# Performance work log

Measured on AMD Instinct MI355X. Metric: run time of the kernel, lower is better.

The kernel has to match this reference:

```python
import jax, jax.numpy as jnp
import numpy as np

B, S, D, H, O = 128, 1024, 64, 512, 1


def setup_inputs() -> dict:
    key = jax.random.key(0)
    ks = jax.random.split(key, 16)
    sc = 1.0 / np.sqrt(H)
    u = lambda k, shape: jax.random.uniform(k, shape, jnp.float32, -sc, sc)
    return {
        "x": jax.random.normal(ks[0], (B, S, D), jnp.float32),
        "W_ih0": u(ks[1], (4 * H, D)), "W_hh0": u(ks[2], (4 * H, H)),
        "b_ih0": u(ks[3], (4 * H,)), "b_hh0": u(ks[4], (4 * H,)),
        "W_ih1": u(ks[5], (4 * H, H)), "W_hh1": u(ks[6], (4 * H, H)),
        "b_ih1": u(ks[7], (4 * H,)), "b_hh1": u(ks[8], (4 * H,)),
        "W_a": u(ks[9], (H, H)), "b_a": u(ks[10], (H,)),
        "v_a": u(ks[11], (1, H)), "b_v": u(ks[12], (1,)),
        "fc_W": u(ks[13], (O, H)), "fc_b": u(ks[14], (O,)),
    }


def lstm_layer(x_sbd, W_ih, W_hh, b_ih, b_hh):
    # x_sbd: [S, B, Din] -> outputs [S, B, H]; PyTorch gate order i,f,g,o
    h0 = jnp.zeros((x_sbd.shape[1], W_hh.shape[1]), x_sbd.dtype)

    def step(carry, x_t):
        h, c = carry
        g = x_t @ W_ih.T + b_ih + h @ W_hh.T + b_hh
        i, f, gg, o = jnp.split(g, 4, axis=-1)
        c = jax.nn.sigmoid(f) * c + jax.nn.sigmoid(i) * jnp.tanh(gg)
        h = jax.nn.sigmoid(o) * jnp.tanh(c)
        return (h, c), h

    _, hs = jax.lax.scan(step, (h0, h0), x_sbd)
    return hs


def entmax15(x):
    # x: [B, S], normalization over axis 1 (faithful to the source's variant)
    n = x.shape[1]
    x = x - jnp.max(x, axis=1, keepdims=True)
    xs = jnp.flip(jnp.sort(x, axis=1), axis=1)  # descending
    csm = jnp.cumsum(xs, axis=1)
    rhos = jnp.arange(1, n + 1, dtype=x.dtype)
    support = rhos * xs - csm + 0.5
    support_thresh = support / rhos
    ssize = jnp.clip(jnp.sum(support > 0, axis=1, keepdims=True), 1, n - 1)
    tau = jnp.take_along_axis(support_thresh, ssize, axis=1)
    d = x - tau
    pos = d > 0
    y = jnp.where(pos, jnp.sqrt(jnp.where(pos, d, 1.0)), 0.0)
    return y / jnp.sum(y, axis=1, keepdims=True)


def reference(x, W_ih0, W_hh0, b_ih0, b_hh0, W_ih1, W_hh1, b_ih1, b_hh1,
              W_a, b_a, v_a, b_v, fc_W, fc_b):
    x_sbd = jnp.transpose(x, (1, 0, 2))  # [S, B, D]
    h1 = lstm_layer(x_sbd, W_ih0, W_hh0, b_ih0, b_hh0)
    h2 = lstm_layer(h1, W_ih1, W_hh1, b_ih1, b_hh1)
    lstm_out = jnp.transpose(h2, (1, 0, 2))  # [B, S, H]
    # additive attention energies: v_a(tanh(W_a(h)))
    e = jnp.einsum('bsh,oh->bso', jnp.tanh(jnp.einsum('bsh,gh->bsg', lstm_out, W_a) + b_a), v_a) + b_v
    att_weights = entmax15(e[..., 0])  # [B, S]
    context = jnp.einsum('bs,bsh->bh', att_weights, lstm_out)
    # dropout is identity in eval mode
    output = context @ fc_W.T + fc_b  # [B, O]
    return output, att_weights
```

## Files before the change

### kernel.cpp

```cpp
#include <hip/hip_runtime.h>

typedef __attribute__((ext_vector_type(8))) _Float16 half8;
typedef __attribute__((ext_vector_type(4))) float f32x4;
typedef __attribute__((ext_vector_type(4))) int   i32x4;

#define DEV static __device__ __forceinline__

DEV i32x4 mfma8i(i32x4 a, i32x4 b, i32x4 c){
  return __builtin_amdgcn_mfma_i32_16x16x64_i8(a, b, c, 0, 0, 0);
}
DEV void ld4(i32x4& d, const char* p){
  asm volatile("global_load_dwordx4 %0, %1, off sc0 sc1" : "=v"(d) : "v"(p));
}
DEV void st1(char* p, int v){
  asm volatile("global_store_byte %0, %1, off sc0 sc1" :: "v"(p), "v"(v) : "memory");
}
DEV void st_flag(unsigned int* p, unsigned int v){
  asm volatile("s_waitcnt vmcnt(0)" ::: "memory");
  asm volatile("global_store_dword %0, %1, off sc0 sc1" :: "v"(p), "v"(v) : "memory");
}
DEV void drain_vm(){ asm volatile("s_waitcnt vmcnt(0)" ::: "memory"); }
DEV void poll_ge(unsigned int* fp, unsigned int tgt){
  for (;;){
    unsigned int v = __hip_atomic_load(fp, __ATOMIC_RELAXED, __HIP_MEMORY_SCOPE_AGENT);
    if (__all(v >= tgt)) break;
    __builtin_amdgcn_s_sleep(1);
  }
}

DEV void str_h(const i32x4* W, const i32x4* B, i32x4* G){
  G[0]=mfma8i(W[0],B[0],G[0]);
  G[1]=mfma8i(W[0],B[1],G[1]); G[1]=mfma8i(W[1],B[0],G[1]);
  G[2]=mfma8i(W[0],B[2],G[2]); G[2]=mfma8i(W[1],B[1],G[2]); G[2]=mfma8i(W[2],B[0],G[2]);
  G[3]=mfma8i(W[0],B[3],G[3]); G[3]=mfma8i(W[1],B[2],G[3]); G[3]=mfma8i(W[2],B[1],G[3]); G[3]=mfma8i(W[3],B[0],G[3]);
  G[4]=mfma8i(W[0],B[4],G[4]); G[4]=mfma8i(W[1],B[3],G[4]); G[4]=mfma8i(W[2],B[2],G[4]); G[4]=mfma8i(W[3],B[1],G[4]); G[4]=mfma8i(W[4],B[0],G[4]);
  G[5]=mfma8i(W[1],B[4],G[5]); G[5]=mfma8i(W[2],B[3],G[5]); G[5]=mfma8i(W[3],B[2],G[5]); G[5]=mfma8i(W[4],B[1],G[5]);
}
DEV void str_x(const i32x4* W, const i32x4* X, i32x4* G){
  G[0]=mfma8i(W[0],X[0],G[0]);
  G[1]=mfma8i(W[0],X[1],G[1]); G[1]=mfma8i(W[1],X[0],G[1]);
  G[2]=mfma8i(W[0],X[2],G[2]); G[2]=mfma8i(W[1],X[1],G[2]); G[2]=mfma8i(W[2],X[0],G[2]);
  G[3]=mfma8i(W[0],X[3],G[3]); G[3]=mfma8i(W[1],X[2],G[3]); G[3]=mfma8i(W[2],X[1],G[3]); G[3]=mfma8i(W[3],X[0],G[3]);
  G[4]=mfma8i(W[0],X[4],G[4]); G[4]=mfma8i(W[1],X[3],G[4]); G[4]=mfma8i(W[2],X[2],G[4]); G[4]=mfma8i(W[3],X[1],G[4]); G[4]=mfma8i(W[4],X[0],G[4]);
  G[5]=mfma8i(W[0],X[5],G[5]); G[5]=mfma8i(W[1],X[4],G[5]); G[5]=mfma8i(W[2],X[3],G[5]); G[5]=mfma8i(W[3],X[2],G[5]); G[5]=mfma8i(W[4],X[1],G[5]);
}

#define SEG_STRIDE 4352
#define NSEG 20
#define LDS_BYTES  (NSEG * SEG_STRIDE)

DEV void stage_issue(char* const* hp, size_t tbase, i32x4* v, int tid){
  const int row = tid >> 4;
  const int off = (tid & 15) * 16;
  #pragma unroll
  for (int u = 0; u < NSEG; ++u){
    int plane = u >> 2, tile = (u >> 1) & 1, half = u & 1;
    ld4(v[u], hp[plane] + tbase + (size_t)(tile * 16 + row) * 512 + (size_t)half * 256 + off);
  }
}
DEV void stage_write(const i32x4* v, char* lds, int tid){
  const int row = tid >> 4;
  const int off = (tid & 15) * 16;
  #pragma unroll
  for (int u = 0; u < NSEG; ++u)
    *(i32x4*)(lds + u * SEG_STRIDE + row * 272 + off) = v[u];
}

DEV void compute_full(const char* const* wp, size_t rowb, int wofs,
                      const char* lds, int l15, int l4, i32x4* Ga, i32x4* Gb){
  #pragma unroll
  for (int c = 0; c < 8; ++c){
    const int half = c >> 2, cc = c & 3;
    i32x4 Wc[5], Ba[5], Bb[5];
    #pragma unroll
    for (int p = 0; p < 5; ++p)
      Wc[p] = *(const i32x4*)(wp[p] + rowb + (size_t)(wofs + c) * 64 + l4 * 16);
    #pragma unroll
    for (int p = 0; p < 5; ++p){
      Ba[p] = *(const i32x4*)(lds + (p * 4 + 0 + half) * SEG_STRIDE + l15 * 272 + cc * 64 + l4 * 16);
      Bb[p] = *(const i32x4*)(lds + (p * 4 + 2 + half) * SEG_STRIDE + l15 * 272 + cc * 64 + l4 * 16);
    }
    str_h(Wc, Ba, Ga);
    str_h(Wc, Bb, Gb);
  }
}

__global__ void k_prep_zero(unsigned int* cnt){
  cnt[threadIdx.x] = 0u;
}

DEV void wsplit5(float v, char* o1, char* o2, char* o3, char* o4, char* o5){
  float q1 = rintf(v * 0x1p11f);
  float r1 = fmaf(q1, -0x1p-11f, v);
  float q2 = rintf(r1 * 0x1p18f);
  float r2 = fmaf(q2, -0x1p-18f, r1);
  float q3 = rintf(r2 * 0x1p25f);
  float r3 = fmaf(q3, -0x1p-25f, r2);
  float q4 = rintf(r3 * 0x1p32f);
  float r4 = fmaf(q4, -0x1p-32f, r3);
  float q5 = rintf(r4 * 0x1p39f);
  *o1=(char)(int)q1; *o2=(char)(int)q2; *o3=(char)(int)q3;
  *o4=(char)(int)q4; *o5=(char)(int)q5;
}

__global__ void k_prep_w0(const float* __restrict__ Wih0, const float* __restrict__ Whh0,
                          char* __restrict__ p1, char* __restrict__ p2, char* __restrict__ p3,
                          char* __restrict__ p4, char* __restrict__ p5){
  int idx = blockIdx.x * 256 + threadIdx.x;
  int k = idx % 576;
  int r = (idx / 576) & 63;
  int j = idx / 36864;
  int R = (r & 3) * 512 + j * 16 + (r >> 2);
  float v = (k < 512) ? Whh0[(size_t)R * 512 + k] : Wih0[(size_t)R * 64 + (k - 512)];
  wsplit5(v, p1 + idx, p2 + idx, p3 + idx, p4 + idx, p5 + idx);
}

__global__ void k_prep_w1(const float* __restrict__ Wih1, const float* __restrict__ Whh1,
                          char* __restrict__ p1, char* __restrict__ p2, char* __restrict__ p3,
                          char* __restrict__ p4, char* __restrict__ p5){
  int idx = blockIdx.x * 256 + threadIdx.x;
  int k = idx & 1023;
  int r = (idx >> 10) & 63;
  int j = idx >> 16;
  int R = (r & 3) * 512 + j * 16 + (r >> 2);
  float v = (k < 512) ? Wih1[(size_t)R * 512 + k] : Whh1[(size_t)R * 512 + (k - 512)];
  wsplit5(v, p1 + idx, p2 + idx, p3 + idx, p4 + idx, p5 + idx);
}

__global__ void k_prep_b(const float* __restrict__ bih0, const float* __restrict__ bhh0,
                         const float* __restrict__ bih1, const float* __restrict__ bhh1,
                         double* __restrict__ bias0, double* __restrict__ bias1){
  int idx = blockIdx.x * 256 + threadIdx.x;
  int i2 = idx & 2047;
  int j = i2 >> 6, r = i2 & 63;
  int R = (r & 3) * 512 + j * 16 + (r >> 2);
  if (idx < 2048) bias0[i2] = (double)bih0[R] + (double)bhh0[R];
  else            bias1[i2] = (double)bih1[R] + (double)bhh1[R];
}

__global__ void k_prep_wa(const float* __restrict__ Wa,
                          char* __restrict__ p1, char* __restrict__ p2,
                          char* __restrict__ p3, char* __restrict__ p4){
  int idx = blockIdx.x * 256 + threadIdx.x;
  float v = Wa[idx];
  float q1 = rintf(v * 0x1p11f);
  float r1 = fmaf(q1, -0x1p-11f, v);
  float q2 = rintf(r1 * 0x1p18f);
  float r2 = fmaf(q2, -0x1p-18f, r1);
  float q3 = rintf(r2 * 0x1p25f);
  float r3 = fmaf(q3, -0x1p-25f, r2);
  float q4 = rintf(r3 * 0x1p32f);
  p1[idx]=(char)(int)q1; p2[idx]=(char)(int)q2;
  p3[idx]=(char)(int)q3; p4[idx]=(char)(int)q4;
}

DEV void hsplit5(double hd, char* o1, char* o2, char* o3, char* o4, char* o5){
  double q1 = rint(hd * 64.0);
  double r1 = hd - q1 * 0x1p-6;
  double q2 = rint(r1 * 0x1p13);
  double r2 = r1 - q2 * 0x1p-13;
  double q3 = rint(r2 * 0x1p20);
  double r3 = r2 - q3 * 0x1p-20;
  double q4 = rint(r3 * 0x1p27);
  double r4 = r3 - q4 * 0x1p-27;
  double q5 = rint(r4 * 0x1p34);
  *o1=(char)(int)q1; *o2=(char)(int)q2; *o3=(char)(int)q3;
  *o4=(char)(int)q4; *o5=(char)(int)q5;
}

DEV double sigd(double xv){ return 1.0 / (1.0 + exp(-xv)); }

__constant__ double SH_[6] = {0x1p-17, 0x1p-24, 0x1p-31, 0x1p-38, 0x1p-45, 0x1p-52};
__constant__ double SX_[6] = {0x1p-13, 0x1p-20, 0x1p-27, 0x1p-34, 0x1p-41, 0x1p-48};

__global__ __launch_bounds__(256, 1) void k_lstm_fused(
    const float* __restrict__ x,
    const char* w0p1, const char* w0p2, const char* w0p3, const char* w0p4, const char* w0p5,
    const double* __restrict__ bias0,
    const char* w1p1, const char* w1p2, const char* w1p3, const char* w1p4, const char* w1p5,
    const double* __restrict__ bias1,
    char* h1a, char* h1b, char* h1c, char* h1d, char* h1e,
    char* h2a, char* h2b, char* h2c, char* h2d, char* h2e,
    _Float16* __restrict__ h2h, char* __restrict__ h2l8,
    unsigned int* __restrict__ cnt)
{
  __shared__ char sbuf[LDS_BYTES];
  const int wg   = blockIdx.x;
  const int tid  = threadIdx.x;
  const int w    = tid >> 6;
  const int lane = tid & 63;
  const int l15  = lane & 15;
  const int l4   = lane >> 4;
  unsigned int* pflagL0 = cnt;
  unsigned int* pflagH2 = cnt + 128;

  const int isL1 = wg >= 128;
  const int wgl  = isL1 ? wg - 128 : wg;
  const int gi   = wgl >> 5;
  const int j    = wgl & 31;
  const int r0   = w * 16 + l15;
  const int b0   = gi * 32 + l15;
  const int b1   = b0 + 16;
  const int hid  = j * 16 + w * 4 + l4;
  const size_t ringmt0 = (size_t)b0 * 512;
  const size_t ringmt1 = (size_t)b1 * 512;
  const size_t gbase   = (size_t)(gi * 32) * 512;

  char* h1p[5] = {h1a, h1b, h1c, h1d, h1e};
  char* h2p[5] = {h2a, h2b, h2c, h2d, h2e};
  const i32x4 z = {0,0,0,0};

  if (!isL1){
    const char* wp[5] = {w0p1, w0p2, w0p3, w0p4, w0p5};
    const size_t rowb = ((size_t)j * 64 + r0) * 576;
    i32x4 WX[5];
    #pragma unroll
    for (int p = 0; p < 5; ++p)
      WX[p] = *(const i32x4*)(wp[p] + rowb + 8 * 64 + l4 * 16);
    double bsd[4];
    #pragma unroll
    for (int q = 0; q < 4; ++q) bsd[q] = bias0[j * 64 + w * 16 + l4 * 4 + q];
    double c0 = 0.0, c1 = 0.0;

    for (int t = 0; t < 1024; ++t){
      i32x4 XA[6], XB[6];
      {
        #pragma unroll
        for (int mt = 0; mt < 2; ++mt){
          const float* xr = x + ((size_t)(mt ? b1 : b0) * 1024 + t) * 64 + l4 * 16;
          unsigned int a[6][4] = {{0,0,0,0},{0,0,0,0},{0,0,0,0},{0,0,0,0},{0,0,0,0},{0,0,0,0}};
          #pragma unroll
          for (int i = 0; i < 16; ++i){
            float v = xr[i];
            float q1 = rintf(v * 4.0f);
            float r1 = fmaf(q1, -0.25f, v);
            float q2 = rintf(r1 * 0x1p9f);
            float r2 = fmaf(q2, -0x1p-9f, r1);
            float q3 = rintf(r2 * 0x1p16f);
            float r3 = fmaf(q3, -0x1p-16f, r2);
            float q4 = rintf(r3 * 0x1p23f);
            float r4 = fmaf(q4, -0x1p-23f, r3);
            float q5 = rintf(r4 * 0x1p30f);
            float r5 = fmaf(q5, -0x1p-30f, r4);
            float q6 = rintf(r5 * 0x1p37f);
            int wi = i >> 2, sh = (i & 3) * 8;
            a[0][wi] |= ((unsigned)(unsigned char)(char)(int)q1) << sh;
            a[1][wi] |= ((unsigned)(unsigned char)(char)(int)q2) << sh;
            a[2][wi] |= ((unsigned)(unsigned char)(char)(int)q3) << sh;
            a[3][wi] |= ((unsigned)(unsigned char)(char)(int)q4) << sh;
            a[4][wi] |= ((unsigned)(unsigned char)(char)(int)q5) << sh;
            a[5][wi] |= ((unsigned)(unsigned char)(char)(int)q6) << sh;
          }
          i32x4* X = mt ? XB : XA;
          #pragma unroll
          for (int p = 0; p < 6; ++p)
            X[p] = i32x4{(int)a[p][0], (int)a[p][1], (int)a[p][2], (int)a[p][3]};
        }
      }
      i32x4 Gha[6], Ghb[6], Gxa[6], Gxb[6];
      #pragma unroll
      for (int k = 0; k < 6; ++k){ Gha[k]=z; Ghb[k]=z; Gxa[k]=z; Gxb[k]=z; }
      str_x(WX, XA, Gxa);
      str_x(WX, XB, Gxb);

      if (w == 0){
        unsigned int* fp = (lane < 32) ? (pflagL0 + gi * 32 + lane)
                                       : (pflagH2 + gi * 32 + (lane - 32));
        unsigned int tgt = (lane < 32) ? (unsigned)t
                          : ((t >= 8) ? (unsigned)(t - 7) : 0u);
        poll_ge(fp, tgt);
      }
      __syncthreads();

      if (t > 0){
        i32x4 A[NSEG];
        const size_t sb = ((size_t)((t - 1) & 7) << 16) + gbase;
        stage_issue(h1p, sb, A, tid);
        drain_vm();
        __builtin_amdgcn_sched_barrier(0);
        stage_write(A, sbuf, tid);
        __syncthreads();
        compute_full(wp, rowb, 0, sbuf, l15, l4, Gha, Ghb);
      }

      const size_t rb = (size_t)(t & 7) << 16;
      #pragma unroll
      for (int mt = 0; mt < 2; ++mt){
        i32x4* Gh = mt ? Ghb : Gha;
        i32x4* Gx = mt ? Gxb : Gxa;
        double g[4];
        #pragma unroll
        for (int q = 0; q < 4; ++q){
          double s = bsd[q];
          #pragma unroll
          for (int k = 0; k < 6; ++k)
            s += (double)Gh[k][q] * SH_[k] + (double)Gx[k][q] * SX_[k];
          g[q] = s;
        }
        double& cs = mt ? c1 : c0;
        cs = sigd(g[1]) * cs + sigd(g[0]) * tanh(g[2]);
        double hv = sigd(g[3]) * tanh(cs);
        size_t o = rb + (mt ? ringmt1 : ringmt0) + hid;
        char v1c, v2c, v3c, v4c, v5c;
        hsplit5(hv, &v1c, &v2c, &v3c, &v4c, &v5c);
        st1(h1p[0] + o, v1c); st1(h1p[1] + o, v2c); st1(h1p[2] + o, v3c);
        st1(h1p[3] + o, v4c); st1(h1p[4] + o, v5c);
      }

      drain_vm();
      __syncthreads();
      if (tid == 0) st_flag(pflagL0 + wgl, (unsigned)(t + 1));
    }
  } else {
    const char* wp[5] = {w1p1, w1p2, w1p3, w1p4, w1p5};
    const size_t rowb = ((size_t)j * 64 + r0) * 1024;
    double bsd[4];
    #pragma unroll
    for (int q = 0; q < 4; ++q) bsd[q] = bias1[j * 64 + w * 16 + l4 * 4 + q];
    double c0 = 0.0, c1 = 0.0;

    for (int t = 0; t < 1024; ++t){
      if (w == 0){
        unsigned int* fp = (lane < 32) ? (pflagL0 + gi * 32 + lane)
                                       : (pflagH2 + gi * 32 + (lane - 32));
        unsigned int tgt = (lane < 32) ? (unsigned)(t + 1)
                          : ((t > 0) ? (unsigned)t : 0u);
        poll_ge(fp, tgt);
      }
      __syncthreads();

      i32x4 Gha[6], Ghb[6];
      #pragma unroll
      for (int k = 0; k < 6; ++k){ Gha[k]=z; Ghb[k]=z; }

      i32x4 A[NSEG], Bv[NSEG];
      const size_t sbA = ((size_t)(t & 7) << 16) + gbase;
      stage_issue(h1p, sbA, A, tid);
      if (t > 0){
        const size_t sbB = ((size_t)((t - 1) & 3) << 16) + gbase;
        stage_issue(h2p, sbB, Bv, tid);
        asm volatile("s_waitcnt vmcnt(20)" ::: "memory");
      } else {
        drain_vm();
      }
      __builtin_amdgcn_sched_barrier(0);
      stage_write(A, sbuf, tid);
      __syncthreads();
      compute_full(wp, rowb, 0, sbuf, l15, l4, Gha, Ghb);
      __syncthreads();

      if (t > 0){
        drain_vm();
        __builtin_amdgcn_sched_barrier(0);
        stage_write(Bv, sbuf, tid);
        __syncthreads();
        compute_full(wp, rowb, 8, sbuf, l15, l4, Gha, Ghb);
      }

      const size_t rb = (size_t)(t & 3) << 16;
      #pragma unroll
      for (int mt = 0; mt < 2; ++mt){
        i32x4* Gh = mt ? Ghb : Gha;
        double g[4];
        #pragma unroll
        for (int q = 0; q < 4; ++q){
          double s = bsd[q];
          #pragma unroll
          for (int k = 0; k < 6; ++k) s += (double)Gh[k][q] * SH_[k];
          g[q] = s;
        }
        double& cs = mt ? c1 : c0;
        cs = sigd(g[1]) * cs + sigd(g[0]) * tanh(g[2]);
        double hv = sigd(g[3]) * tanh(cs);
        size_t o = rb + (mt ? ringmt1 : ringmt0) + hid;
        char v1c, v2c, v3c, v4c, v5c;
        hsplit5(hv, &v1c, &v2c, &v3c, &v4c, &v5c);
        st1(h2p[0] + o, v1c); st1(h2p[1] + o, v2c); st1(h2p[2] + o, v3c);
        st1(h2p[3] + o, v4c); st1(h2p[4] + o, v5c);
        float hf = (float)hv;
        _Float16 hh = (_Float16)hf;
        float rs = hf - (float)hh;
        union { _Float16 h; unsigned short u; } cb; cb.h = hh;
        int E = (cb.u >> 10) & 31; if (E < 1) E = 1;
        int qr = (int)rintf(ldexpf(rs, 33 - E));
        qr = qr < -127 ? -127 : (qr > 127 ? 127 : qr);
        size_t pb = ((size_t)(mt ? b1 : b0) * 1024 + t) * 512 + hid;
        h2h[pb] = hh;
        h2l8[pb] = (char)qr;
      }

      drain_vm();
      __syncthreads();
      if (tid == 0) st_flag(pflagH2 + wgl, (unsigned)(t + 1));
    }
  }
}

__global__ __launch_bounds__(256) void k_att_e(
    const _Float16* __restrict__ h2, const char* __restrict__ h2l8,
    const char* __restrict__ wa1, const char* __restrict__ wa2,
    const char* __restrict__ wa3, const char* __restrict__ wa4,
    const float* __restrict__ b_a, const float* __restrict__ v_a,
    const float* __restrict__ b_v, double* __restrict__ e)
{
  __shared__ char Ap[4][32][528];
  __shared__ char Wp[2][4][16][528];
  __shared__ double partial[2][32];
  const int tid  = threadIdx.x;
  const int w    = tid >> 6;
  const int mt   = w & 1;
  const int nh   = w >> 1;
  const int lane = tid & 63;
  const int l15  = lane & 15;
  const int l4   = lane >> 4;
  const size_t rid0 = (size_t)blockIdx.x * 32;

  for (int i = tid; i < 2048; i += 256){
    int row = i >> 6, c8 = (i & 63) << 3;
    const _Float16* hp = h2 + (rid0 + row) * 512 + c8;
    const char*     rp = h2l8 + (rid0 + row) * 512 + c8;
    unsigned long long o1 = 0, o2 = 0, o3 = 0, o4 = 0;
    #pragma unroll
    for (int q = 0; q < 8; ++q){
      union { _Float16 h; unsigned short u; } cb; cb.h = hp[q];
      int E = (cb.u >> 10) & 31; if (E < 1) E = 1;
      float h = (float)cb.h + ldexpf((float)rp[q], E - 33);
      float q1 = rintf(h * 64.f);     float r1 = fmaf(q1, -0x1p-6f, h);
      float q2 = rintf(r1 * 0x1p13f); float r2 = fmaf(q2, -0x1p-13f, r1);
      float q3 = rintf(r2 * 0x1p20f); float r3 = fmaf(q3, -0x1p-20f, r2);
      float q4 = rintf(r3 * 0x1p27f);
      o1 |= ((unsigned long long)(unsigned char)(char)(int)q1) << (8 * q);
      o2 |= ((unsigned long long)(unsigned char)(char)(int)q2) << (8 * q);
      o3 |= ((unsigned long long)(unsigned char)(char)(int)q3) << (8 * q);
      o4 |= ((unsigned long long)(unsigned char)(char)(int)q4) << (8 * q);
    }
    *(unsigned long long*)&Ap[0][row][c8] = o1;
    *(unsigned long long*)&Ap[1][row][c8] = o2;
    *(unsigned long long*)&Ap[2][row][c8] = o3;
    *(unsigned long long*)&Ap[3][row][c8] = o4;
  }
  __syncthreads();

  const int sh = tid >> 7;
  const int st = tid & 127;
  double ep0 = 0.0, ep1 = 0.0, ep2 = 0.0, ep3 = 0.0;
  for (int it = 0; it < 16; ++it){
    if (it) __syncthreads();
    {
      int nt = sh * 16 + it;
      for (int i = st; i < 512; i += 128){
        int row = (i >> 5) & 15, c16 = (i & 31) << 4;
        size_t go = (size_t)(nt * 16 + row) * 512 + c16;
        *(i32x4*)&Wp[sh][0][row][c16] = *(const i32x4*)(wa1 + go);
        *(i32x4*)&Wp[sh][1][row][c16] = *(const i32x4*)(wa2 + go);
        *(i32x4*)&Wp[sh][2][row][c16] = *(const i32x4*)(wa3 + go);
        *(i32x4*)&Wp[sh][3][row][c16] = *(const i32x4*)(wa4 + go);
      }
    }
    __syncthreads();
    i32x4 G0={0,0,0,0},G1={0,0,0,0},G2={0,0,0,0},G3={0,0,0,0},G4={0,0,0,0},G5={0,0,0,0};
    #pragma unroll
    for (int c = 0; c < 8; ++c){
      int ko = c * 64 + l4 * 16;
      i32x4 A1 = *(const i32x4*)&Ap[0][mt * 16 + l15][ko];
      i32x4 A2 = *(const i32x4*)&Ap[1][mt * 16 + l15][ko];
      i32x4 A3 = *(const i32x4*)&Ap[2][mt * 16 + l15][ko];
      i32x4 A4 = *(const i32x4*)&Ap[3][mt * 16 + l15][ko];
      i32x4 B1 = *(const i32x4*)&Wp[nh][0][l15][ko];
      i32x4 B2 = *(const i32x4*)&Wp[nh][1][l15][ko];
      i32x4 B3 = *(const i32x4*)&Wp[nh][2][l15][ko];
      i32x4 B4 = *(const i32x4*)&Wp[nh][3][l15][ko];
      G0 = mfma8i(A1, B1, G0);
      G1 = mfma8i(A1, B2, G1); G1 = mfma8i(A2, B1, G1);
      G2 = mfma8i(A1, B3, G2); G2 = mfma8i(A2, B2, G2); G2 = mfma8i(A3, B1, G2);
      G3 = mfma8i(A1, B4, G3); G3 = mfma8i(A2, B3, G3); G3 = mfma8i(A3, B2, G3); G3 = mfma8i(A4, B1, G3);
      G4 = mfma8i(A2, B4, G4); G4 = mfma8i(A3, B3, G4); G4 = mfma8i(A4, B2, G4);
      G5 = mfma8i(A3, B4, G5); G5 = mfma8i(A4, B3, G5);
    }
    int n = (nh * 16 + it) * 16 + l15;
    double ban = (double)b_a[n], van = (double)v_a[n];
    #pragma unroll
    for (int q = 0; q < 4; ++q){
      double val = (double)G0[q]*SH_[0] + (double)G1[q]*SH_[1] + (double)G2[q]*SH_[2]
                 + (double)G3[q]*SH_[3] + (double)G4[q]*SH_[4] + (double)G5[q]*SH_[5] + ban;
      double tv = tanh(val) * van;
      if (q == 0) ep0 += tv; else if (q == 1) ep1 += tv;
      else if (q == 2) ep2 += tv; else ep3 += tv;
    }
  }
  #pragma unroll
  for (int m = 1; m < 16; m <<= 1){
    ep0 += __shfl_xor(ep0, m); ep1 += __shfl_xor(ep1, m);
    ep2 += __shfl_xor(ep2, m); ep3 += __shfl_xor(ep3, m);
  }
  if (l15 == 0){
    int rbase = mt * 16 + l4 * 4;
    partial[nh][rbase + 0] = ep0;
    partial[nh][rbase + 1] = ep1;
    partial[nh][rbase + 2] = ep2;
    partial[nh][rbase + 3] = ep3;
  }
  __syncthreads();
  if (tid < 32)
    e[rid0 + tid] = partial[0][tid] + partial[1][tid] + (double)b_v[0];
}

__global__ __launch_bounds__(256) void k_entmax(
    const double* __restrict__ e, const _Float16* __restrict__ h2,
    const float* __restrict__ fcW, const float* __restrict__ fcb,
    float* __restrict__ out)
{
  __shared__ double xu[1024], sbd[1024], t0d[1024], t1d[1024];
  __shared__ float sbf[1024];
  __shared__ float red4[4];
  __shared__ double redd[4];
  __shared__ double scald;
  const int tid  = threadIdx.x;
  const int b    = blockIdx.x;
  const int wv   = tid >> 6;
  const int lane = tid & 63;

  double lm = -1e300;
  for (int i = tid; i < 1024; i += 256){
    double v = e[b * 1024 + i];
    xu[i] = v;
    lm = fmax(lm, v);
  }
  for (int m = 32; m >= 1; m >>= 1) lm = fmax(lm, __shfl_xor(lm, m));
  if (lane == 0) redd[wv] = lm;
  __syncthreads();
  double rowmax = fmax(fmax(redd[0], redd[1]), fmax(redd[2], redd[3]));
  __syncthreads();
  for (int i = tid; i < 1024; i += 256){
    double v = xu[i] - rowmax;
    xu[i] = v; sbd[i] = v;
  }
  __syncthreads();

  for (int ksz = 2; ksz <= 1024; ksz <<= 1){
    for (int jj = ksz >> 1; jj > 0; jj >>= 1){
      for (int i = tid; i < 1024; i += 256){
        int ixj = i ^ jj;
        if (ixj > i){
          double a = sbd[i], c = sbd[ixj];
          if (((i & ksz) == 0) ? (a > c) : (a < c)){ sbd[i] = c; sbd[ixj] = a; }
        }
      }
      __syncthreads();
    }
  }

  for (int i = tid; i < 1024; i += 256) t0d[i] = sbd[1023 - i];
  __syncthreads();
  double* src = t0d; double* dst = t1d;
  for (int off = 1; off < 1024; off <<= 1){
    for (int i = tid; i < 1024; i += 256)
      dst[i] = src[i] + ((i >= off) ? src[i - off] : 0.0);
    __syncthreads();
    double* tmp = src; src = dst; dst = tmp;
  }

  float lc = 0.f;
  for (int i = tid; i < 1024; i += 256){
    double xs_i = sbd[1023 - i];
    double sup = (double)(i + 1) * xs_i - src[i] + 0.5;
    if (sup > 0.0) lc += 1.f;
  }
  for (int m = 32; m >= 1; m >>= 1) lc += __shfl_xor(lc, m);
  if (lane == 0) red4[wv] = lc;
  __syncthreads();
  if (tid == 0){
    int cntS = (int)(red4[0] + red4[1] + red4[2] + red4[3] + 0.5f);
    int ss = cntS < 1 ? 1 : (cntS > 1023 ? 1023 : cntS);
    double xss = sbd[1023 - ss];
    scald = ((double)(ss + 1) * xss - src[ss] + 0.5) / (double)(ss + 1);
  }
  __syncthreads();
  double tau = scald;

  double ls = 0.0;
  for (int i = tid; i < 1024; i += 256){
    double d = xu[i] - tau;
    double y = (d > 0.0) ? sqrt(d) : 0.0;
    dst[i] = y;
    ls += y;
  }
  for (int m = 32; m >= 1; m >>= 1) ls += __shfl_xor(ls, m);
  if (lane == 0) redd[wv] = ls;
  __syncthreads();
  double Z = redd[0] + redd[1] + redd[2] + redd[3];
  __syncthreads();
  for (int i = tid; i < 1024; i += 256){
    float a = (float)(dst[i] / Z);
    sbf[i] = a;
    out[128 + b * 1024 + i] = a;
  }
  __syncthreads();

  const int h0 = tid * 2;
  float cx0 = 0.f, cx1 = 0.f;
  for (int s = 0; s < 1024; ++s){
    float wt = sbf[s];
    if (wt > 0.f){
      unsigned int u = *(const unsigned int*)(h2 + ((size_t)b * 1024 + s) * 512 + h0);
      union { unsigned int u; _Float16 h[2]; } cv; cv.u = u;
      cx0 += wt * (float)cv.h[0];
      cx1 += wt * (float)cv.h[1];
    }
  }
  float p = fcW[h0] * cx0 + fcW[h0 + 1] * cx1;
  for (int m = 32; m >= 1; m >>= 1) p += __shfl_xor(p, m);
  if (lane == 0) red4[wv] = p;
  __syncthreads();
  if (tid == 0) out[b] = red4[0] + red4[1] + red4[2] + red4[3] + fcb[0];
}

extern "C" void kernel_launch(void* const* d_in, const int* in_sizes, int n_in,
                              void* d_out, int out_size, void* d_ws, size_t ws_size,
                              hipStream_t stream)
{
  (void)in_sizes; (void)n_in; (void)out_size;
  const float* x    = (const float*)d_in[0];
  const float* Wih0 = (const float*)d_in[1];
  const float* Whh0 = (const float*)d_in[2];
  const float* bih0 = (const float*)d_in[3];
  const float* bhh0 = (const float*)d_in[4];
  const float* Wih1 = (const float*)d_in[5];
  const float* Whh1 = (const float*)d_in[6];
  const float* bih1 = (const float*)d_in[7];
  const float* bhh1 = (const float*)d_in[8];
  const float* Wa   = (const float*)d_in[9];
  const float* ba   = (const float*)d_in[10];
  const float* va   = (const float*)d_in[11];
  const float* bv   = (const float*)d_in[12];
  const float* fcW  = (const float*)d_in[13];
  const float* fcb  = (const float*)d_in[14];

  const size_t NEED = 223773696ull;
  if (ws_size < NEED) return;

  char* ws = (char*)d_ws;
  unsigned int* cnt = (unsigned int*)(ws);
  char* w0p[5]; for (int p = 0; p < 5; ++p) w0p[p] = ws + 1024ull + (size_t)p * 1179648ull;
  double* bias0 = (double*)(ws + 5899264ull);
  char* w1p[5]; for (int p = 0; p < 5; ++p) w1p[p] = ws + 5915648ull + (size_t)p * 2097152ull;
  double* bias1 = (double*)(ws + 16401408ull);
  char* wa1 = ws + 16417792ull;
  char* wa2 = wa1 + 262144ull;
  char* wa3 = wa2 + 262144ull;
  char* wa4 = wa3 + 262144ull;
  char* h1p[5]; for (int p = 0; p < 5; ++p) h1p[p] = ws + 17466368ull + (size_t)p * 524288ull;
  char* h2p[5]; for (int p = 0; p < 5; ++p) h2p[p] = ws + 20087808ull + (size_t)p * 262144ull;
  double* ebuf = (double*)(ws + 21398528ull);
  _Float16* h2h = (_Float16*)(ws + 22447104ull);
  char* h2l8 = ws + 156664832ull;
  float* out = (float*)d_out;

  k_prep_zero<<<1, 256, 0, stream>>>(cnt);
  k_prep_w0<<<4608, 256, 0, stream>>>(Wih0, Whh0, w0p[0], w0p[1], w0p[2], w0p[3], w0p[4]);
  k_prep_w1<<<8192, 256, 0, stream>>>(Wih1, Whh1, w1p[0], w1p[1], w1p[2], w1p[3], w1p[4]);
  k_prep_b<<<16, 256, 0, stream>>>(bih0, bhh0, bih1, bhh1, bias0, bias1);
  k_prep_wa<<<1024, 256, 0, stream>>>(Wa, wa1, wa2, wa3, wa4);
  k_lstm_fused<<<256, 256, 0, stream>>>(x,
      w0p[0], w0p[1], w0p[2], w0p[3], w0p[4], bias0,
      w1p[0], w1p[1], w1p[2], w1p[3], w1p[4], bias1,
      h1p[0], h1p[1], h1p[2], h1p[3], h1p[4],
      h2p[0], h2p[1], h2p[2], h2p[3], h2p[4],
      h2h, h2l8, cnt);
  k_att_e<<<4096, 256, 0, stream>>>(h2h, h2l8, wa1, wa2, wa3, wa4, ba, va, bv, ebuf);
  k_entmax<<<128, 256, 0, stream>>>(ebuf, h2h, fcW, fcb, out);
}
```

Before: 19.41 ms.

## Repartition LSTM work: 16-batch groups, two gate tiles per wave sharing B-operand

Reassigns the persistent LSTM workgroups so each covers 16 batch rows (8 batch groups) and two 16-row weight tiles per wave, instead of 32 batch rows with one weight tile. Each LDS B fragment is now reused across two weight tiles, and the per-step staging of the hidden state halves (NSEG 20→10). Layer 0 now polls its dependency flags before doing the x-projection. The intent is to shrink per-step staging and LDS traffic and reduce the number of flags polled on the serial recurrence critical path. In exchange each wave loads twice as many weight fragments, and the layer-0 x-projection no longer overlaps the flag wait.

```diff
diff --git a/kernel.cpp b/kernel.cpp
--- a/kernel.cpp
+++ b/kernel.cpp
@@ -46,7 +46,7 @@
 }
 
 #define SEG_STRIDE 4352
-#define NSEG 20
+#define NSEG 10
 #define LDS_BYTES  (NSEG * SEG_STRIDE)
 
 DEV void stage_issue(char* const* hp, size_t tbase, i32x4* v, int tid){
@@ -54,8 +54,8 @@
   const int off = (tid & 15) * 16;
   #pragma unroll
   for (int u = 0; u < NSEG; ++u){
-    int plane = u >> 2, tile = (u >> 1) & 1, half = u & 1;
-    ld4(v[u], hp[plane] + tbase + (size_t)(tile * 16 + row) * 512 + (size_t)half * 256 + off);
+    int plane = u >> 1, half = u & 1;
+    ld4(v[u], hp[plane] + tbase + (size_t)row * 512 + (size_t)half * 256 + off);
   }
 }
 DEV void stage_write(const i32x4* v, char* lds, int tid){
@@ -66,22 +66,23 @@
     *(i32x4*)(lds + u * SEG_STRIDE + row * 272 + off) = v[u];
 }
 
-DEV void compute_full(const char* const* wp, size_t rowb, int wofs,
-                      const char* lds, int l15, int l4, i32x4* Ga, i32x4* Gb){
+DEV void compute_phase(const char* const* wp, size_t rowbA, size_t rowbB, size_t K,
+                       int wofs, const char* lds, int l15, int l4,
+                       i32x4* Ga, i32x4* Gb){
   #pragma unroll
   for (int c = 0; c < 8; ++c){
     const int half = c >> 2, cc = c & 3;
-    i32x4 Wc[5], Ba[5], Bb[5];
+    i32x4 WcA[5], WcB[5], Ba[5];
+    #pragma unroll
+    for (int p = 0; p < 5; ++p){
+      WcA[p] = *(const i32x4*)(wp[p] + rowbA + (size_t)(wofs + c) * 64 + l4 * 16);
+      WcB[p] = *(const i32x4*)(wp[p] + rowbB + (size_t)(wofs + c) * 64 + l4 * 16);
+    }
     #pragma unroll
     for (int p = 0; p < 5; ++p)
-      Wc[p] = *(const i32x4*)(wp[p] + rowb + (size_t)(wofs + c) * 64 + l4 * 16);
-    #pragma unroll
-    for (int p = 0; p < 5; ++p){
-      Ba[p] = *(const i32x4*)(lds + (p * 4 + 0 + half) * SEG_STRIDE + l15 * 272 + cc * 64 + l4 * 16);
-      Bb[p] = *(const i32x4*)(lds + (p * 4 + 2 + half) * SEG_STRIDE + l15 * 272 + cc * 64 + l4 * 16);
-    }
-    str_h(Wc, Ba, Ga);
-    str_h(Wc, Bb, Gb);
+      Ba[p] = *(const i32x4*)(lds + (p * 2 + half) * SEG_STRIDE + l15 * 272 + cc * 64 + l4 * 16);
+    str_h(WcA, Ba, Ga);
+    str_h(WcB, Ba, Gb);
   }
 }
 
@@ -191,20 +192,20 @@
   const int lane = tid & 63;
   const int l15  = lane & 15;
   const int l4   = lane >> 4;
+
+  const int gi    = wg & 7;
+  const int m     = wg >> 3;
+  const int isL1  = m & 1;
+  const int j     = m >> 1;
+  const int s     = 2 * j + (w >> 1);
+  const int rbase = (w & 1) * 32;
+  const int rA    = rbase + l15;
+  const int batch = gi * 16 + l15;
+  const int hidA  = s * 16 + (w & 1) * 8 + l4;
+  const size_t gbase = (size_t)(gi * 16) * 512;
   unsigned int* pflagL0 = cnt;
   unsigned int* pflagH2 = cnt + 128;
-
-  const int isL1 = wg >= 128;
-  const int wgl  = isL1 ? wg - 128 : wg;
-  const int gi   = wgl >> 5;
-  const int j    = wgl & 31;
-  const int r0   = w * 16 + l15;
-  const int b0   = gi * 32 + l15;
-  const int b1   = b0 + 16;
-  const int hid  = j * 16 + w * 4 + l4;
-  const size_t ringmt0 = (size_t)b0 * 512;
-  const size_t ringmt1 = (size_t)b1 * 512;
-  const size_t gbase   = (size_t)(gi * 32) * 512;
+  const int myflag = gi * 16 + j;
 
   char* h1p[5] = {h1a, h1b, h1c, h1d, h1e};
   char* h2p[5] = {h2a, h2b, h2c, h2d, h2e};
@@ -212,75 +213,80 @@
 
   if (!isL1){
     const char* wp[5] = {w0p1, w0p2, w0p3, w0p4, w0p5};
-    const size_t rowb = ((size_t)j * 64 + r0) * 576;
-    i32x4 WX[5];
-    #pragma unroll
-    for (int p = 0; p < 5; ++p)
-      WX[p] = *(const i32x4*)(wp[p] + rowb + 8 * 64 + l4 * 16);
-    double bsd[4];
-    #pragma unroll
-    for (int q = 0; q < 4; ++q) bsd[q] = bias0[j * 64 + w * 16 + l4 * 4 + q];
+    const size_t rowbA = ((size_t)s * 64 + rA) * 576;
+    const size_t rowbB = rowbA + 16 * 576;
+    i32x4 WXA[5], WXB[5];
+    #pragma unroll
+    for (int p = 0; p < 5; ++p){
+      WXA[p] = *(const i32x4*)(wp[p] + rowbA + 8 * 64 + l4 * 16);
+      WXB[p] = *(const i32x4*)(wp[p] + rowbB + 8 * 64 + l4 * 16);
+    }
+    double bsdA[4], bsdB[4];
+    #pragma unroll
+    for (int q = 0; q < 4; ++q){
+      bsdA[q] = bias0[s * 64 + rbase + l4 * 4 + q];
+      bsdB[q] = bias0[s * 64 + rbase + 16 + l4 * 4 + q];
+    }
     double c0 = 0.0, c1 = 0.0;
 
     for (int t = 0; t < 1024; ++t){
-      i32x4 XA[6], XB[6];
+      if (w == 0){
+        unsigned int* fp; unsigned int tgt;
+        if (lane < 16){ fp = pflagL0 + gi * 16 + lane; tgt = (unsigned)t; }
+        else if (lane < 32){ fp = pflagH2 + gi * 16 + (lane - 16); tgt = (t >= 8) ? (unsigned)(t - 7) : 0u; }
+        else { fp = pflagL0; tgt = 0u; }
+        poll_ge(fp, tgt);
+      }
+      __syncthreads();
+
+      i32x4 A[NSEG];
+      if (t > 0){
+        const size_t sb = ((size_t)((t - 1) & 7) << 16) + gbase;
+        stage_issue(h1p, sb, A, tid);
+      }
+
+      i32x4 X[6];
       {
+        const float* xr = x + ((size_t)batch * 1024 + t) * 64 + l4 * 16;
+        unsigned int a[6][4] = {{0,0,0,0},{0,0,0,0},{0,0,0,0},{0,0,0,0},{0,0,0,0},{0,0,0,0}};
         #pragma unroll
-        for (int mt = 0; mt < 2; ++mt){
-          const float* xr = x + ((size_t)(mt ? b1 : b0) * 1024 + t) * 64 + l4 * 16;
-          unsigned int a[6][4] = {{0,0,0,0},{0,0,0,0},{0,0,0,0},{0,0,0,0},{0,0,0,0},{0,0,0,0}};
-          #pragma unroll
-          for (int i = 0; i < 16; ++i){
-            float v = xr[i];
-            float q1 = rintf(v * 4.0f);
-            float r1 = fmaf(q1, -0.25f, v);
-            float q2 = rintf(r1 * 0x1p9f);
-            float r2 = fmaf(q2, -0x1p-9f, r1);
-            float q3 = rintf(r2 * 0x1p16f);
-            float r3 = fmaf(q3, -0x1p-16f, r2);
-            float q4 = rintf(r3 * 0x1p23f);
-            float r4 = fmaf(q4, -0x1p-23f, r3);
-            float q5 = rintf(r4 * 0x1p30f);
-            float r5 = fmaf(q5, -0x1p-30f, r4);
-            float q6 = rintf(r5 * 0x1p37f);
-            int wi = i >> 2, sh = (i & 3) * 8;
-            a[0][wi] |= ((unsigned)(unsigned char)(char)(int)q1) << sh;
-            a[1][wi] |= ((unsigned)(unsigned char)(char)(int)q2) << sh;
-            a[2][wi] |= ((unsigned)(unsigned char)(char)(int)q3) << sh;
-            a[3][wi] |= ((unsigned)(unsigned char)(char)(int)q4) << sh;
-            a[4][wi] |= ((unsigned)(unsigned char)(char)(int)q5) << sh;
-            a[5][wi] |= ((unsigned)(unsigned char)(char)(int)q6) << sh;
-          }
-          i32x4* X = mt ? XB : XA;
-          #pragma unroll
-          for (int p = 0; p < 6; ++p)
-            X[p] = i32x4{(int)a[p][0], (int)a[p][1], (int)a[p][2], (int)a[p][3]};
+        for (int i = 0; i < 16; ++i){
+          float v = xr[i];
+          float q1 = rintf(v * 4.0f);
+          float r1 = fmaf(q1, -0.25f, v);
+          float q2 = rintf(r1 * 0x1p9f);
+          float r2 = fmaf(q2, -0x1p-9f, r1);
+          float q3 = rintf(r2 * 0x1p16f);
+          float r3 = fmaf(q3, -0x1p-16f, r2);
+          float q4 = rintf(r3 * 0x1p23f);
+          float r4 = fmaf(q4, -0x1p-23f, r3);
+          float q5 = rintf(r4 * 0x1p30f);
+          float r5 = fmaf(q5, -0x1p-30f, r4);
+          float q6 = rintf(r5 * 0x1p37f);
+          int wi = i >> 2, sh = (i & 3) * 8;
+          a[0][wi] |= ((unsigned)(unsigned char)(char)(int)q1) << sh;
+          a[1][wi] |= ((unsigned)(unsigned char)(char)(int)q2) << sh;
+          a[2][wi] |= ((unsigned)(unsigned char)(char)(int)q3) << sh;
+          a[3][wi] |= ((unsigned)(unsigned char)(char)(int)q4) << sh;
+          a[4][wi] |= ((unsigned)(unsigned char)(char)(int)q5) << sh;
+          a[5][wi] |= ((unsigned)(unsigned char)(char)(int)q6) << sh;
         }
+        #pragma unroll
+        for (int p = 0; p < 6; ++p)
+          X[p] = i32x4{(int)a[p][0], (int)a[p][1], (int)a[p][2], (int)a[p][3]};
       }
       i32x4 Gha[6], Ghb[6], Gxa[6], Gxb[6];
       #pragma unroll
       for (int k = 0; k < 6; ++k){ Gha[k]=z; Ghb[k]=z; Gxa[k]=z; Gxb[k]=z; }
-      str_x(WX, XA, Gxa);
-      str_x(WX, XB, Gxb);
-
-      if (w == 0){
-        unsigned int* fp = (lane < 32) ? (pflagL0 + gi * 32 + lane)
-                                       : (pflagH2 + gi * 32 + (lane - 32));
-        unsigned int tgt = (lane < 32) ? (unsigned)t
-                          : ((t >= 8) ? (unsigned)(t - 7) : 0u);
-        poll_ge(fp, tgt);
-      }
-      __syncthreads();
+      str_x(WXA, X, Gxa);
+      str_x(WXB, X, Gxb);
 
       if (t > 0){
-        i32x4 A[NSEG];
-        const size_t sb = ((size_t)((t - 1) & 7) << 16) + gbase;
-        stage_issue(h1p, sb, A, tid);
         drain_vm();
         __builtin_amdgcn_sched_barrier(0);
         stage_write(A, sbuf, tid);
         __syncthreads();
-        compute_full(wp, rowb, 0, sbuf, l15, l4, Gha, Ghb);
+        compute_phase(wp, rowbA, rowbB, 576, 0, sbuf, l15, l4, Gha, Ghb);
       }
 
       const size_t rb = (size_t)(t & 7) << 16;
@@ -288,19 +294,20 @@
       for (int mt = 0; mt < 2; ++mt){
         i32x4* Gh = mt ? Ghb : Gha;
         i32x4* Gx = mt ? Gxb : Gxa;
+        double* bsd = mt ? bsdB : bsdA;
         double g[4];
         #pragma unroll
         for (int q = 0; q < 4; ++q){
-          double s = bsd[q];
+          double sacc = bsd[q];
           #pragma unroll
           for (int k = 0; k < 6; ++k)
-            s += (double)Gh[k][q] * SH_[k] + (double)Gx[k][q] * SX_[k];
-          g[q] = s;
+            sacc += (double)Gh[k][q] * SH_[k] + (double)Gx[k][q] * SX_[k];
+          g[q] = sacc;
         }
         double& cs = mt ? c1 : c0;
         cs = sigd(g[1]) * cs + sigd(g[0]) * tanh(g[2]);
         double hv = sigd(g[3]) * tanh(cs);
-        size_t o = rb + (mt ? ringmt1 : ringmt0) + hid;
+        size_t o = rb + (size_t)batch * 512 + (hidA + mt * 4);
         char v1c, v2c, v3c, v4c, v5c;
         hsplit5(hv, &v1c, &v2c, &v3c, &v4c, &v5c);
         st1(h1p[0] + o, v1c); st1(h1p[1] + o, v2c); st1(h1p[2] + o, v3c);
@@ -309,22 +316,26 @@
 
       drain_vm();
       __syncthreads();
-      if (tid == 0) st_flag(pflagL0 + wgl, (unsigned)(t + 1));
+      if (tid == 0) st_flag(pflagL0 + myflag, (unsigned)(t + 1));
     }
   } else {
     const char* wp[5] = {w1p1, w1p2, w1p3, w1p4, w1p5};
-    const size_t rowb = ((size_t)j * 64 + r0) * 1024;
-    double bsd[4];
-    #pragma unroll
-    for (int q = 0; q < 4; ++q) bsd[q] = bias1[j * 64 + w * 16 + l4 * 4 + q];
+    const size_t rowbA = ((size_t)s * 64 + rA) * 1024;
+    const size_t rowbB = rowbA + 16 * 1024;
+    double bsdA[4], bsdB[4];
+    #pragma unroll
+    for (int q = 0; q < 4; ++q){
+      bsdA[q] = bias1[s * 64 + rbase + l4 * 4 + q];
+      bsdB[q] = bias1[s * 64 + rbase + 16 + l4 * 4 + q];
+    }
     double c0 = 0.0, c1 = 0.0;
 
     for (int t = 0; t < 1024; ++t){
       if (w == 0){
-        unsigned int* fp = (lane < 32) ? (pflagL0 + gi * 32 + lane)
-                                       : (pflagH2 + gi * 32 + (lane - 32));
-        unsigned int tgt = (lane < 32) ? (unsigned)(t + 1)
-                          : ((t > 0) ? (unsigned)t : 0u);
+        unsigned int* fp; unsigned int tgt;
+        if (lane < 16){ fp = pflagL0 + gi * 16 + lane; tgt = (unsigned)(t + 1); }
+        else if (lane < 32){ fp = pflagH2 + gi * 16 + (lane - 16); tgt = (t > 0) ? (unsigned)t : 0u; }
+        else { fp = pflagL0; tgt = 0u; }
         poll_ge(fp, tgt);
       }
       __syncthreads();
@@ -339,14 +350,14 @@
       if (t > 0){
         const size_t sbB = ((size_t)((t - 1) & 3) << 16) + gbase;
         stage_issue(h2p, sbB, Bv, tid);
-        asm volatile("s_waitcnt vmcnt(20)" ::: "memory");
+        asm volatile("s_waitcnt vmcnt(10)" ::: "memory");
       } else {
         drain_vm();
       }
       __builtin_amdgcn_sched_barrier(0);
       stage_write(A, sbuf, tid);
       __syncthreads();
-      compute_full(wp, rowb, 0, sbuf, l15, l4, Gha, Ghb);
+      compute_phase(wp, rowbA, rowbB, 1024, 0, sbuf, l15, l4, Gha, Ghb);
       __syncthreads();
 
       if (t > 0){
@@ -354,25 +365,27 @@
         __builtin_amdgcn_sched_barrier(0);
         stage_write(Bv, sbuf, tid);
         __syncthreads();
-        compute_full(wp, rowb, 8, sbuf, l15, l4, Gha, Ghb);
+        compute_phase(wp, rowbA, rowbB, 1024, 8, sbuf, l15, l4, Gha, Ghb);
       }
 
       const size_t rb = (size_t)(t & 3) << 16;
       #pragma unroll
       for (int mt = 0; mt < 2; ++mt){
         i32x4* Gh = mt ? Ghb : Gha;
+        double* bsd = mt ? bsdB : bsdA;
         double g[4];
         #pragma unroll
         for (int q = 0; q < 4; ++q){
-          double s = bsd[q];
+          double sacc = bsd[q];
           #pragma unroll
-          for (int k = 0; k < 6; ++k) s += (double)Gh[k][q] * SH_[k];
-          g[q] = s;
+          for (int k = 0; k < 6; ++k) sacc += (double)Gh[k][q] * SH_[k];
+          g[q] = sacc;
         }
         double& cs = mt ? c1 : c0;
         cs = sigd(g[1]) * cs + sigd(g[0]) * tanh(g[2]);
         double hv = sigd(g[3]) * tanh(cs);
-        size_t o = rb + (mt ? ringmt1 : ringmt0) + hid;
+        const int hid = hidA + mt * 4;
+        size_t o = rb + (size_t)batch * 512 + hid;
         char v1c, v2c, v3c, v4c, v5c;
         hsplit5(hv, &v1c, &v2c, &v3c, &v4c, &v5c);
         st1(h2p[0] + o, v1c); st1(h2p[1] + o, v2c); st1(h2p[2] + o, v3c);
@@ -384,14 +397,14 @@
         int E = (cb.u >> 10) & 31; if (E < 1) E = 1;
         int qr = (int)rintf(ldexpf(rs, 33 - E));
         qr = qr < -127 ? -127 : (qr > 127 ? 127 : qr);
-        size_t pb = ((size_t)(mt ? b1 : b0) * 1024 + t) * 512 + hid;
+        size_t pb = ((size_t)batch * 1024 + t) * 512 + hid;
         h2h[pb] = hh;
         h2l8[pb] = (char)qr;
       }
 
       drain_vm();
       __syncthreads();
-      if (tid == 0) st_flag(pflagH2 + wgl, (unsigned)(t + 1));
+      if (tid == 0) st_flag(pflagH2 + myflag, (unsigned)(t + 1));
     }
   }
 }
```

After: 34.76 ms. 1.79x slower.
